# Performance work log

Hardware: AMD Instinct MI355X
Metric: run time of the kernel (lower is better)

Reference implementation:

```python
import jax, jax.numpy as jnp
import numpy as np


def _glorot(key, shape):
    lim = np.sqrt(6.0 / (shape[-2] + shape[-1])).astype(np.float32)
    return jax.random.uniform(key, shape, jnp.float32, -lim, lim)


def setup_inputs() -> dict:
    key = jax.random.key(0)
    B, F, K, L = 8192, 256, 32768, 4
    H = 2 * F          # CouplingLayer(feat_size, feat_size * 2) hidden width
    half = F // 2      # affine coupling transforms half the features
    ks = jax.random.split(key, 6)
    return {
        "inputs": jax.random.normal(ks[0], (B, F), jnp.float32),
        "W1": _glorot(ks[1], (L, half, H)),
        "b1": jnp.zeros((L, H), jnp.float32),
        "Ws": _glorot(ks[2], (L, H, half)),
        "bs": jnp.zeros((L, half), jnp.float32),
        "Wt": _glorot(ks[3], (L, H, half)),
        "bt": jnp.zeros((L, half), jnp.float32),
        "prior": _glorot(ks[4], (K, F)),  # VQ codebook, GlorotUniform init as in source
    }


def _forward_flow(x, W1, b1, Ws, bs, Wt, bt):
    """Stack of affine coupling layers; returns (y, log|det J|) per sample."""
    L = W1.shape[0]
    jac = jnp.zeros((x.shape[0],), x.dtype)
    for l in range(L):  # small fixed layer count
        xa, xb = jnp.split(x, 2, axis=1)                 # [B, F/2] each
        h = jax.nn.relu(xa @ W1[l] + b1[l])              # [B, 2F]
        s_raw = h @ Ws[l] + bs[l]                        # [B, F/2]
        s = s_raw if l == L - 1 else jnp.tanh(s_raw)     # last layer: tf.identity
        t = h @ Wt[l] + bt[l]
        yb = xb * jnp.exp(s) + t
        jac = jac + jnp.sum(s, axis=1)
        x = jnp.concatenate([yb, xa], axis=1)            # swap halves for mixing
    return x, jac


def reference(inputs, W1, b1, Ws, bs, Wt, bt, prior):
    sg = jax.lax.stop_gradient
    x, jac = _forward_flow(inputs, W1, b1, Ws, bs, Wt, bt)   # [B, F], [B]
    # pairwise squared distance to codebook: [B, K]
    na = jnp.sum(x * x, axis=1, keepdims=True)               # [B, 1]
    nb = jnp.sum(prior * prior, axis=1)[None, :]             # [1, K]
    d = jnp.maximum(na - 2.0 * (x @ prior.T) + nb, 0.0)      # [B, K]
    target_ind = jnp.argmin(d, axis=1)                       # [B]
    target = prior[target_ind]                               # gather, [B, F]
    loss_1 = jnp.mean(jnp.sum((x - sg(target)) ** 2, axis=1) / 2)
    loss_2 = jnp.mean(jnp.sum((sg(x) - target) ** 2, axis=1) / 2)
    loss = loss_1 + 0.25 * loss_2 - jnp.mean(jac)
    return x, loss
```

## Files before the change

kernel.cpp:

```cpp
#include <hip/hip_runtime.h>
#include <stdint.h>

#define NB     8192
#define NF     256
#define NHALF  128
#define NHID   512
#define NLAY   4
#define NK     32768

typedef __attribute__((ext_vector_type(8))) short bf16x8;
typedef __attribute__((ext_vector_type(4))) float f32x4;

static __device__ __forceinline__ unsigned short f2bf(float f) {
  union { float f; unsigned int u; } v; v.f = f;
  return (unsigned short)((v.u + 0x7FFFu + ((v.u >> 16) & 1u)) >> 16);
}
static __device__ __forceinline__ float bf2f(unsigned short u) {
  union { unsigned int u; float f; } v; v.u = ((unsigned int)u) << 16; return v.f;
}

static __device__ __forceinline__ void load_lds16(const void* g, void* l) {
  __builtin_amdgcn_global_load_lds(
      (const __attribute__((address_space(1))) unsigned int*)g,
      (__attribute__((address_space(3))) unsigned int*)l, 16, 0, 0);
}

static __device__ __forceinline__ unsigned long long packsi(float v, int idx) {
  unsigned int b = __float_as_uint(v);
  b = (b & 0x80000000u) ? ~b : (b | 0x80000000u);
  return ((unsigned long long)b << 32) | (unsigned int)(~(unsigned int)idx);
}

static __device__ __forceinline__ float fast_tanh(float x) {
  const float xc = fminf(fmaxf(x, -15.f), 15.f);
  const float e2 = __expf(2.f * xc);
  return 1.f - 2.f / (e2 + 1.f);
}

static __device__ __forceinline__ int swadr(int kseg, int nrows, int row, int kin) {
  return (kseg * nrows + row) * 64 + (((kin >> 3) ^ (row & 7)) * 8) + (kin & 7);
}

__global__ __launch_bounds__(256, 2)
void flow_all(const float* __restrict__ in,
              const unsigned short* __restrict__ W1T,
              const unsigned short* __restrict__ W2I,
              const float* __restrict__ b1A,
              const float* __restrict__ bsA,
              const float* __restrict__ btA,
              float* __restrict__ xout,
              unsigned short* __restrict__ xfbf,
              float* __restrict__ jac)
{
  __shared__ __align__(16) unsigned short Xb[2][16 * 128];
  __shared__ __align__(16) unsigned short Hs[2 * 16 * 64];
  __shared__ __align__(16) unsigned short Bs[2048 * 8];
  __shared__ float jlds[3][16];
  const int tid = threadIdx.x;
  const int lane = tid & 63, wave = tid >> 6;
  const int q = lane >> 4, c = lane & 15;
  const int m0 = blockIdx.x * 16;

#pragma unroll
  for (int v = 0; v < 4; v++) {
    const int t4 = tid + v * 256;
    const int row = t4 >> 6, f4 = t4 & 63;
    const float4 d = *(const float4*)(in + (size_t)(m0 + row) * NF + f4 * 4);
    unsigned short* dst = Xb[f4 >> 5];
    const int feat = (f4 & 31) * 4;
    const float vals[4] = {d.x, d.y, d.z, d.w};
#pragma unroll
    for (int u = 0; u < 4; u++) {
      const int fe = feat + u;
      dst[swadr(fe >> 6, 16, row, fe & 63)] = f2bf(vals[u]);
    }
  }

  float jr[4];
#pragma unroll
  for (int r = 0; r < 4; r++) jr[r] = 0.f;

  for (int l = 0; l < NLAY; l++) {
    __syncthreads();
    const unsigned short* W1l = W1T + (size_t)l * NHID * NHALF;
    const unsigned short* W2l = W2I + (size_t)l * NF * NHID;
    const float* b1l = b1A + l * NHID;
    const float* bsl = bsA + l * NHALF;
    const float* btl = btA + l * NHALF;
    unsigned short* XA = Xb[l & 1];
    unsigned short* XB = Xb[1 - (l & 1)];

    bf16x8 af1[4];
#pragma unroll
    for (int kw = 0; kw < 4; kw++) {
      const int kch = kw * 4 + q;
      af1[kw] = *(const bf16x8*)(XA + ((kch >> 3) * 16 + c) * 64 +
                                 (((kch & 7) ^ (c & 7)) * 8));
    }

    const f32x4 z = {0.f, 0.f, 0.f, 0.f};
    f32x4 acc2[4];
#pragma unroll
    for (int j = 0; j < 4; j++) acc2[j] = z;

    for (int nc = 0; nc < 4; nc++) {
      __syncthreads();
#pragma unroll
      for (int u = 0; u < 8; u++) {
        const int chb = (wave * 8 + u) * 64;
        const int ch = chb + lane;
        const int kseg = ch >> 10, cs = ch & 1023;
        const int row = cs >> 3, cc = (cs & 7) ^ (row & 7);
        load_lds16(W1l + (size_t)(nc * 128 + row) * NHALF + kseg * 64 + cc * 8,
                   Bs + chb * 8);
      }
      __syncthreads();

      f32x4 acc1[2];
#pragma unroll
      for (int j = 0; j < 2; j++) acc1[j] = z;

#pragma unroll
      for (int kw = 0; kw < 4; kw++) {
        const int kseg = kw >> 1, g = (kw & 1) * 4 + q;
#pragma unroll
        for (int j = 0; j < 2; j++) {
          const int rb = wave * 32 + 16 * j + c;
          const bf16x8 bf = *(const bf16x8*)(Bs + (kseg * 128 + rb) * 64 + ((g ^ (rb & 7)) * 8));
          acc1[j] = __builtin_amdgcn_mfma_f32_16x16x32_bf16(af1[kw], bf, acc1[j], 0, 0, 0);
        }
      }
#pragma unroll
      for (int j = 0; j < 2; j++) {
        const int hc = wave * 32 + 16 * j + c;
        const float bb = b1l[nc * 128 + hc];
#pragma unroll
        for (int r = 0; r < 4; r++) {
          float v = acc1[j][r] + bb;
          v = v > 0.f ? v : 0.f;
          Hs[swadr(hc >> 6, 16, 4 * q + r, hc & 63)] = f2bf(v);
        }
      }

      for (int kt2 = 0; kt2 < 2; kt2++) {
        __syncthreads();
#pragma unroll
        for (int u = 0; u < 8; u++) {
          const int chb = (wave * 8 + u) * 64;
          const int ch = chb + lane;
          const int row = ch >> 3, cc = (ch & 7) ^ (row & 7);
          load_lds16(W2l + (size_t)row * NHID + nc * 128 + kt2 * 64 + cc * 8,
                     Bs + chb * 8);
        }
        __syncthreads();
#pragma unroll
        for (int ks = 0; ks < 2; ks++) {
          const int g = ks * 4 + q;
          const bf16x8 afh = *(const bf16x8*)(Hs + (kt2 * 16 + c) * 64 + ((g ^ (c & 7)) * 8));
#pragma unroll
          for (int j = 0; j < 4; j++) {
            const int rb = wave * 64 + 16 * j + c;
            const bf16x8 bf = *(const bf16x8*)(Bs + rb * 64 + ((g ^ (rb & 7)) * 8));
            acc2[j] = __builtin_amdgcn_mfma_f32_16x16x32_bf16(afh, bf, acc2[j], 0, 0, 0);
          }
        }
      }
    }

    const int parity = c & 1;
    const int lastl = (l == NLAY - 1);
#pragma unroll
    for (int j = 0; j < 4; j++) {
      const int col = wave * 64 + 16 * j + c;
#pragma unroll
      for (int r = 0; r < 4; r++) {
        const float val = acc2[j][r];
        const float oth = __shfl_xor(val, 1);
        if (!parity) {
          const int feat = col >> 1;
          float s = val + bsl[feat];
          if (!lastl) s = fast_tanh(s);
          const float t = oth + btl[feat];
          const int row = 4 * q + r;
          const int xaddr = swadr(feat >> 6, 16, row, feat & 63);
          const float xb = bf2f(XB[xaddr]);
          const float yb = xb * __expf(s) + t;
          jr[r] += s;
          XB[xaddr] = f2bf(yb);
          const size_t grow = (size_t)(m0 + row) * NF;
          if (l == 2) { xout[grow + NHALF + feat] = yb; xfbf[grow + NHALF + feat] = f2bf(yb); }
          if (lastl)  { xout[grow + feat] = yb;         xfbf[grow + feat] = f2bf(yb); }
        }
      }
    }
  }

  float v0[4];
#pragma unroll
  for (int r = 0; r < 4; r++) {
    float v = jr[r];
    v += __shfl_xor(v, 1); v += __shfl_xor(v, 2);
    v += __shfl_xor(v, 4); v += __shfl_xor(v, 8);
    if (c == 0) {
      if (wave) jlds[wave - 1][4 * q + r] = v;
      else v0[r] = v;
    }
  }
  __syncthreads();
  if (wave == 0 && c == 0) {
#pragma unroll
    for (int r = 0; r < 4; r++) {
      const int row = 4 * q + r;
      jac[m0 + row] = v0[r] + jlds[0][row] + jlds[1][row] + jlds[2][row];
    }
  }
}

__global__ __launch_bounds__(256, 2)
void vq_argmax(const unsigned short* __restrict__ X,
               const unsigned short* __restrict__ P,
               const float* __restrict__ nbh,
               unsigned long long* __restrict__ gbest)
{
  __shared__ __align__(16) unsigned short Bs[4 * 64 * 64];
  const int tid = threadIdx.x;
  const int lane = tid & 63, wave = tid >> 6;
  const int y = blockIdx.x & 15;
  const int m0 = (blockIdx.x >> 4) * 256;
  const int q = lane >> 4, c = lane & 15;
  const int mw = m0 + wave * 64;

  bf16x8 af[4][8];
#pragma unroll
  for (int i = 0; i < 4; i++) {
    const unsigned short* xr = X + (size_t)(mw + 16 * i + c) * 256 + q * 8;
#pragma unroll
    for (int kc = 0; kc < 8; kc++) af[i][kc] = *(const bf16x8*)(xr + kc * 32);
  }

  float bestv[16];
  int besti[16];
#pragma unroll
  for (int t = 0; t < 16; t++) { bestv[t] = -1e30f; besti[t] = 0; }

  for (int nt = 0; nt < 32; nt++) {
    const int n0 = y * 2048 + nt * 64;
    if (nt) __syncthreads();
#pragma unroll
    for (int u = 0; u < 8; u++) {
      const int chb = (wave * 8 + u) * 64;
      const int ch = chb + lane;
      const int kseg = ch >> 9, cs = ch & 511;
      const int row = cs >> 3, cc = (cs & 7) ^ (row & 7);
      load_lds16(P + (size_t)(n0 + row) * 256 + kseg * 64 + cc * 8, Bs + chb * 8);
    }
    __syncthreads();

    const f32x4 z = {0.f, 0.f, 0.f, 0.f};
    f32x4 acc[4][4];
#pragma unroll
    for (int i = 0; i < 4; i++)
#pragma unroll
      for (int j = 0; j < 4; j++) acc[i][j] = z;

#pragma unroll
    for (int kseg = 0; kseg < 4; kseg++)
#pragma unroll
      for (int ks = 0; ks < 2; ks++) {
        const int kc = kseg * 2 + ks;
        const int g = ks * 4 + q;
#pragma unroll
        for (int j = 0; j < 4; j++) {
          const int rb = 16 * j + c;
          const bf16x8 bf = *(const bf16x8*)(Bs + (kseg * 64 + rb) * 64 + ((g ^ (rb & 7)) * 8));
          acc[0][j] = __builtin_amdgcn_mfma_f32_16x16x32_bf16(af[0][kc], bf, acc[0][j], 0, 0, 0);
          acc[1][j] = __builtin_amdgcn_mfma_f32_16x16x32_bf16(af[1][kc], bf, acc[1][j], 0, 0, 0);
          acc[2][j] = __builtin_amdgcn_mfma_f32_16x16x32_bf16(af[2][kc], bf, acc[2][j], 0, 0, 0);
          acc[3][j] = __builtin_amdgcn_mfma_f32_16x16x32_bf16(af[3][kc], bf, acc[3][j], 0, 0, 0);
        }
      }

#pragma unroll
    for (int j = 0; j < 4; j++) {
      const int col = n0 + 16 * j + c;
      const float nb = nbh[col];
#pragma unroll
      for (int i = 0; i < 4; i++)
#pragma unroll
        for (int r = 0; r < 4; r++) {
          const float sc = acc[i][j][r] - nb;
          const int t = i * 4 + r;
          if (sc > bestv[t]) { bestv[t] = sc; besti[t] = col; }
        }
    }
  }

#pragma unroll
  for (int t = 0; t < 16; t++) {
    float lv = bestv[t]; int li = besti[t];
#pragma unroll
    for (int mk = 8; mk >= 1; mk >>= 1) {
      const float ov = __shfl_xor(lv, mk);
      const int oi = __shfl_xor(li, mk);
      if (ov > lv || (ov == lv && oi < li)) { lv = ov; li = oi; }
    }
    if (c == 0) {
      const int row = mw + 16 * (t >> 2) + q * 4 + (t & 3);
      atomicMax(&gbest[row], packsi(lv, li));
    }
  }
}

__global__ void prep_all(const float* __restrict__ W1,
                         const float* __restrict__ Ws,
                         const float* __restrict__ Wt,
                         const float* __restrict__ prior,
                         unsigned short* __restrict__ W1T,
                         unsigned short* __restrict__ W2I,
                         unsigned short* __restrict__ pbf,
                         float* __restrict__ nbh,
                         unsigned long long* __restrict__ gbest,
                         float* __restrict__ accum)
{
  __shared__ float ts[64 * 65];
  const int bx = blockIdx.x;
  const int tid = threadIdx.x;
  if (bx < 2048) {
    const int k = bx * 16 + (tid >> 4);
    const int l16 = tid & 15;
    float s = 0.f;
#pragma unroll
    for (int v = 0; v < 4; v++) {
      const int off = (v * 16 + l16) * 4;
      const float4 d = *(const float4*)(prior + (size_t)k * NF + off);
      ushort4 o;
      o.x = f2bf(d.x); o.y = f2bf(d.y); o.z = f2bf(d.z); o.w = f2bf(d.w);
      *(ushort4*)(pbf + (size_t)k * NF + off) = o;
      s += d.x * d.x + d.y * d.y + d.z * d.z + d.w * d.w;
    }
#pragma unroll
    for (int mk = 8; mk >= 1; mk >>= 1) s += __shfl_xor(s, mk);
    if (l16 == 0) nbh[k] = 0.5f * s;
  } else if (bx < 2112) {
    const int job = bx - 2048;
    const int l = job >> 4, t = job & 15;
    const int k0 = (t >> 3) * 64, n0 = (t & 7) * 64;
    const float* src = W1 + (size_t)l * NHALF * NHID;
#pragma unroll
    for (int v = 0; v < 16; v++) {
      const int e = tid + v * 256;
      const int kk = e >> 6, nn = e & 63;
      ts[kk * 65 + nn] = src[(size_t)(k0 + kk) * NHID + n0 + nn];
    }
    __syncthreads();
    unsigned short* dst = W1T + (size_t)l * NHID * NHALF;
#pragma unroll
    for (int v = 0; v < 16; v++) {
      const int e = tid + v * 256;
      const int nn = e >> 6, kk = e & 63;
      dst[(size_t)(n0 + nn) * NHALF + k0 + kk] = f2bf(ts[kk * 65 + nn]);
    }
  } else if (bx < 2240) {
    const int job = bx - 2112;
    const int l = job >> 5, rem = job & 31;
    const int b = rem >> 4;
    const int k0 = ((rem >> 1) & 7) * 64;
    const int f0 = (rem & 1) * 64;
    const float* src = (b ? Wt : Ws) + (size_t)l * NHID * NHALF;
#pragma unroll
    for (int v = 0; v < 16; v++) {
      const int e = tid + v * 256;
      const int kk = e >> 6, nn = e & 63;
      ts[kk * 65 + nn] = src[(size_t)(k0 + kk) * NHALF + f0 + nn];
    }
    __syncthreads();
#pragma unroll
    for (int v = 0; v < 16; v++) {
      const int e = tid + v * 256;
      const int nn = e >> 6, kk = e & 63;
      W2I[((size_t)l * NF + 2 * (f0 + nn) + b) * NHID + k0 + kk] = f2bf(ts[kk * 65 + nn]);
    }
  } else {
    const int idx = (bx - 2240) * 256 + tid;
    if (idx < NB) gbest[idx] = 0ull;
    if (idx < 2) accum[idx] = 0.f;
  }
}

__global__ void vq_finalize(const float* __restrict__ X,
                            const float* __restrict__ prior,
                            const unsigned long long* __restrict__ gbest,
                            const float* __restrict__ jac,
                            float* __restrict__ accum)
{
  const int wave = threadIdx.x >> 6, lane = threadIdx.x & 63;
  const int gw = blockIdx.x * 4 + wave;
  float accd = 0.f, accj = 0.f;
  for (int r = 0; r < 8; r++) {
    const int row = gw * 8 + r;
    const unsigned int idx = ~(unsigned int)(gbest[row]);
    const float* x = X + (size_t)row * NF;
    const float* p = prior + (size_t)idx * NF;
#pragma unroll
    for (int u = 0; u < 4; u++) {
      const int d = lane + u * 64;
      const float df = x[d] - p[d];
      accd += df * df;
    }
    if (lane == 0) accj += jac[row];
  }
#pragma unroll
  for (int mk = 32; mk >= 1; mk >>= 1) {
    accd += __shfl_xor(accd, mk);
    accj += __shfl_xor(accj, mk);
  }
  __shared__ float sd[4], sj[4];
  if (lane == 0) { sd[wave] = accd; sj[wave] = accj; }
  __syncthreads();
  if (threadIdx.x == 0) {
    atomicAdd(&accum[0], sd[0] + sd[1] + sd[2] + sd[3]);
    atomicAdd(&accum[1], sj[0] + sj[1] + sj[2] + sj[3]);
  }
}

__global__ void finalize_loss(const float* __restrict__ acc, float* __restrict__ loss) {
  if (threadIdx.x == 0 && blockIdx.x == 0)
    loss[0] = 1.25f * (0.5f * acc[0] / (float)NB) - acc[1] / (float)NB;
}

extern "C" void kernel_launch(void* const* d_in, const int* in_sizes, int n_in,
                              void* d_out, int out_size, void* d_ws, size_t ws_size,
                              hipStream_t stream)
{
  (void)in_sizes; (void)n_in; (void)out_size; (void)ws_size;
  const float* inputs = (const float*)d_in[0];
  const float* W1 = (const float*)d_in[1];
  const float* b1 = (const float*)d_in[2];
  const float* Ws = (const float*)d_in[3];
  const float* bs = (const float*)d_in[4];
  const float* Wt = (const float*)d_in[5];
  const float* bt = (const float*)d_in[6];
  const float* prior = (const float*)d_in[7];

  char* p = (char*)d_ws;
  auto alloc = [&](size_t bytes) { char* r = p; p += (bytes + 255) & ~(size_t)255; return r; };
  unsigned short* W1T  = (unsigned short*)alloc((size_t)NLAY * NHID * NHALF * 2);
  unsigned short* W2I  = (unsigned short*)alloc((size_t)NLAY * NF * NHID * 2);
  unsigned short* PBF  = (unsigned short*)alloc((size_t)NK * NF * 2);
  float* NBH           = (float*)alloc((size_t)NK * 4);
  unsigned short* XFBF = (unsigned short*)alloc((size_t)NB * NF * 2);
  float* JAC           = (float*)alloc((size_t)NB * 4);
  unsigned long long* GBEST = (unsigned long long*)alloc((size_t)NB * 8);
  float* ACC           = (float*)alloc(256);

  float* xout = (float*)d_out;
  float* loss = xout + (size_t)NB * NF;

  prep_all<<<dim3(2272), 256, 0, stream>>>(
      W1, Ws, Wt, prior, W1T, W2I, PBF, NBH, GBEST, ACC);

  flow_all<<<dim3(NB / 16), 256, 0, stream>>>(
      inputs, W1T, W2I, b1, bs, bt, xout, XFBF, JAC);

  vq_argmax<<<dim3(32 * 16), 256, 0, stream>>>(XFBF, PBF, NBH, GBEST);
  vq_finalize<<<dim3(256), 256, 0, stream>>>(xout, prior, GBEST, JAC, ACC);
  finalize_loss<<<1, 1, 0, stream>>>(ACC, loss);
}
```

Before: 293.6 us.

## Use FP8 codebook distance GEMM and software-pipeline flow weight loads

The VQ distance GEMM switches from bf16 to fp8 e4m3 MFMA. Both the flow output and the codebook are scaled and quantized, with a K permutation so the 64-bit fragments load contiguously, which halves codebook bytes and doubles MFMA throughput. The flow kernel is restructured into a flat 96-step schedule with double-buffered LDS weight tiles, prefetching the next tile while the current one computes and cutting barriers. The risk is that fp8 precision flips argmin choices between close codebook entries, changing the selected targets and the loss.

```diff
diff --git a/kernel.cpp b/kernel.cpp
--- a/kernel.cpp
+++ b/kernel.cpp
@@ -1,4 +1,5 @@
 #include <hip/hip_runtime.h>
+#include <hip/hip_fp8.h>
 #include <stdint.h>
 
 #define NB     8192
@@ -8,8 +9,12 @@
 #define NLAY   4
 #define NK     32768
 
+#define SX     (1.0f / 16.0f)
+#define SP     (256.0f)
+
 typedef __attribute__((ext_vector_type(8))) short bf16x8;
 typedef __attribute__((ext_vector_type(4))) float f32x4;
+typedef __attribute__((ext_vector_type(2))) long i64x2;
 
 static __device__ __forceinline__ unsigned short f2bf(float f) {
   union { float f; unsigned int u; } v; v.f = f;
@@ -17,6 +22,16 @@
 }
 static __device__ __forceinline__ float bf2f(unsigned short u) {
   union { unsigned int u; float f; } v; v.u = ((unsigned int)u) << 16; return v.f;
+}
+static __device__ __forceinline__ unsigned char f2fp8(float f) {
+  __hip_fp8_e4m3 q(f);
+  return (unsigned char)q.__x;
+}
+static __device__ __forceinline__ float fp82f(unsigned char b) {
+  __hip_fp8_e4m3 q; q.__x = b; return (float)q;
+}
+static __device__ __forceinline__ int kperm(int k) {
+  return ((k >> 3) & 3) * 64 + ((k >> 5) << 3) + (k & 7);
 }
 
 static __device__ __forceinline__ void load_lds16(const void* g, void* l) {
@@ -49,17 +64,29 @@
               const float* __restrict__ bsA,
               const float* __restrict__ btA,
               float* __restrict__ xout,
-              unsigned short* __restrict__ xfbf,
+              unsigned char* __restrict__ xf8,
               float* __restrict__ jac)
 {
   __shared__ __align__(16) unsigned short Xb[2][16 * 128];
-  __shared__ __align__(16) unsigned short Hs[2 * 16 * 64];
-  __shared__ __align__(16) unsigned short Bs[2048 * 8];
+  __shared__ __align__(16) unsigned short Hs[16 * 64];
+  __shared__ __align__(16) unsigned short Bs[2][8192];
   __shared__ float jlds[3][16];
   const int tid = threadIdx.x;
   const int lane = tid & 63, wave = tid >> 6;
   const int q = lane >> 4, c = lane & 15;
   const int m0 = blockIdx.x * 16;
+
+  {
+    const unsigned short* W1l = W1T;
+#pragma unroll
+    for (int u = 0; u < 4; u++) {
+      const int chb = (u * 4 + wave) * 64;
+      const int ch = chb + lane;
+      const int kseg = ch >> 9, cs = ch & 511;
+      const int row = cs >> 3, cc = (cs & 7) ^ (row & 7);
+      load_lds16(W1l + (size_t)row * 128 + kseg * 64 + cc * 8, Bs[0] + chb * 8);
+    }
+  }
 
 #pragma unroll
   for (int v = 0; v < 4; v++) {
@@ -76,120 +103,114 @@
     }
   }
 
-  float jr[4];
-#pragma unroll
-  for (int r = 0; r < 4; r++) jr[r] = 0.f;
-
-  for (int l = 0; l < NLAY; l++) {
+  float jr[4] = {0.f, 0.f, 0.f, 0.f};
+  bf16x8 af1[4];
+  const f32x4 z = {0.f, 0.f, 0.f, 0.f};
+  f32x4 acc2[4];
+
+  for (int gs = 0; gs < 96; gs++) {
     __syncthreads();
-    const unsigned short* W1l = W1T + (size_t)l * NHID * NHALF;
-    const unsigned short* W2l = W2I + (size_t)l * NF * NHID;
-    const float* b1l = b1A + l * NHID;
-    const float* bsl = bsA + l * NHALF;
-    const float* btl = btA + l * NHALF;
+
+    if (gs + 1 < 96) {
+      const int g2 = gs + 1;
+      const int l2 = g2 / 24, s2 = g2 % 24, nc2 = s2 / 3, t2 = s2 % 3;
+      unsigned short* dst = Bs[g2 & 1];
+      if (t2 == 0) {
+        const unsigned short* W1l = W1T + (size_t)l2 * (NHID * NHALF) + (size_t)nc2 * 64 * 128;
+#pragma unroll
+        for (int u = 0; u < 4; u++) {
+          const int chb = (u * 4 + wave) * 64;
+          const int ch = chb + lane;
+          const int kseg = ch >> 9, cs = ch & 511;
+          const int row = cs >> 3, cc = (cs & 7) ^ (row & 7);
+          load_lds16(W1l + (size_t)row * 128 + kseg * 64 + cc * 8, dst + chb * 8);
+        }
+      } else {
+        const unsigned short* W2l = W2I + (size_t)l2 * (NF * NHID) + nc2 * 64 + (t2 - 1) * 32;
+#pragma unroll
+        for (int u = 0; u < 4; u++) {
+          const int chb = (u * 4 + wave) * 64;
+          const int ch = chb + lane;
+          const int row = ch >> 2;
+          const int cc = (ch & 3) ^ ((row >> 1) & 3);
+          load_lds16(W2l + (size_t)row * NHID + cc * 8, dst + chb * 8);
+        }
+      }
+    }
+
+    const int l = gs / 24, s = gs % 24, nc8 = s / 3, typ = s % 3;
+    const unsigned short* B = Bs[gs & 1];
     unsigned short* XA = Xb[l & 1];
     unsigned short* XB = Xb[1 - (l & 1)];
 
-    bf16x8 af1[4];
-#pragma unroll
-    for (int kw = 0; kw < 4; kw++) {
-      const int kch = kw * 4 + q;
-      af1[kw] = *(const bf16x8*)(XA + ((kch >> 3) * 16 + c) * 64 +
-                                 (((kch & 7) ^ (c & 7)) * 8));
-    }
-
-    const f32x4 z = {0.f, 0.f, 0.f, 0.f};
-    f32x4 acc2[4];
-#pragma unroll
-    for (int j = 0; j < 4; j++) acc2[j] = z;
-
-    for (int nc = 0; nc < 4; nc++) {
-      __syncthreads();
-#pragma unroll
-      for (int u = 0; u < 8; u++) {
-        const int chb = (wave * 8 + u) * 64;
-        const int ch = chb + lane;
-        const int kseg = ch >> 10, cs = ch & 1023;
-        const int row = cs >> 3, cc = (cs & 7) ^ (row & 7);
-        load_lds16(W1l + (size_t)(nc * 128 + row) * NHALF + kseg * 64 + cc * 8,
-                   Bs + chb * 8);
-      }
-      __syncthreads();
-
-      f32x4 acc1[2];
-#pragma unroll
-      for (int j = 0; j < 2; j++) acc1[j] = z;
-
+    if (typ == 0) {
+      if (s == 0) {
+#pragma unroll
+        for (int kw = 0; kw < 4; kw++) {
+          const int kch = kw * 4 + q;
+          af1[kw] = *(const bf16x8*)(XA + ((kch >> 3) * 16 + c) * 64 +
+                                     (((kch & 7) ^ (c & 7)) * 8));
+        }
+#pragma unroll
+        for (int j = 0; j < 4; j++) acc2[j] = z;
+      }
+      f32x4 acc1 = z;
+      const int rb = wave * 16 + c;
 #pragma unroll
       for (int kw = 0; kw < 4; kw++) {
         const int kseg = kw >> 1, g = (kw & 1) * 4 + q;
-#pragma unroll
-        for (int j = 0; j < 2; j++) {
-          const int rb = wave * 32 + 16 * j + c;
-          const bf16x8 bf = *(const bf16x8*)(Bs + (kseg * 128 + rb) * 64 + ((g ^ (rb & 7)) * 8));
-          acc1[j] = __builtin_amdgcn_mfma_f32_16x16x32_bf16(af1[kw], bf, acc1[j], 0, 0, 0);
-        }
-      }
-#pragma unroll
-      for (int j = 0; j < 2; j++) {
-        const int hc = wave * 32 + 16 * j + c;
-        const float bb = b1l[nc * 128 + hc];
+        const bf16x8 bf = *(const bf16x8*)(B + (kseg * 64 + rb) * 64 + ((g ^ (rb & 7)) * 8));
+        acc1 = __builtin_amdgcn_mfma_f32_16x16x32_bf16(af1[kw], bf, acc1, 0, 0, 0);
+      }
+      const int hc = wave * 16 + c;
+      const float bb = b1A[l * NHID + nc8 * 64 + hc];
+#pragma unroll
+      for (int r = 0; r < 4; r++) {
+        float v = acc1[r] + bb;
+        v = v > 0.f ? v : 0.f;
+        Hs[swadr(0, 16, 4 * q + r, hc)] = f2bf(v);
+      }
+    } else {
+      const int half = typ - 1;
+      const bf16x8 afh = *(const bf16x8*)(Hs + c * 64 + (((half * 4 + q) ^ (c & 7)) * 8));
+#pragma unroll
+      for (int j = 0; j < 4; j++) {
+        const int rb = wave * 64 + 16 * j + c;
+        const bf16x8 bf = *(const bf16x8*)(B + rb * 32 + ((q ^ ((rb >> 1) & 3)) * 8));
+        acc2[j] = __builtin_amdgcn_mfma_f32_16x16x32_bf16(afh, bf, acc2[j], 0, 0, 0);
+      }
+    }
+
+    if (s == 23) {
+      const int parity = c & 1;
+      const int lastl = (l == NLAY - 1);
+      const float* bsl = bsA + l * NHALF;
+      const float* btl = btA + l * NHALF;
+#pragma unroll
+      for (int j = 0; j < 4; j++) {
+        const int col = wave * 64 + 16 * j + c;
 #pragma unroll
         for (int r = 0; r < 4; r++) {
-          float v = acc1[j][r] + bb;
-          v = v > 0.f ? v : 0.f;
-          Hs[swadr(hc >> 6, 16, 4 * q + r, hc & 63)] = f2bf(v);
-        }
-      }
-
-      for (int kt2 = 0; kt2 < 2; kt2++) {
-        __syncthreads();
-#pragma unroll
-        for (int u = 0; u < 8; u++) {
-          const int chb = (wave * 8 + u) * 64;
-          const int ch = chb + lane;
-          const int row = ch >> 3, cc = (ch & 7) ^ (row & 7);
-          load_lds16(W2l + (size_t)row * NHID + nc * 128 + kt2 * 64 + cc * 8,
-                     Bs + chb * 8);
-        }
-        __syncthreads();
-#pragma unroll
-        for (int ks = 0; ks < 2; ks++) {
-          const int g = ks * 4 + q;
-          const bf16x8 afh = *(const bf16x8*)(Hs + (kt2 * 16 + c) * 64 + ((g ^ (c & 7)) * 8));
-#pragma unroll
-          for (int j = 0; j < 4; j++) {
-            const int rb = wave * 64 + 16 * j + c;
-            const bf16x8 bf = *(const bf16x8*)(Bs + rb * 64 + ((g ^ (rb & 7)) * 8));
-            acc2[j] = __builtin_amdgcn_mfma_f32_16x16x32_bf16(afh, bf, acc2[j], 0, 0, 0);
+          const float val = acc2[j][r];
+          const float oth = __shfl_xor(val, 1);
+          if (!parity) {
+            const int feat = col >> 1;
+            float sv = val + bsl[feat];
+            if (!lastl) sv = fast_tanh(sv);
+            const float t = oth + btl[feat];
+            const int row = 4 * q + r;
+            const int xaddr = swadr(feat >> 6, 16, row, feat & 63);
+            const float xb = bf2f(XB[xaddr]);
+            const float yb = xb * __expf(sv) + t;
+            jr[r] += sv;
+            XB[xaddr] = f2bf(yb);
+            if (l >= 2) {
+              const int k = lastl ? feat : (NHALF + feat);
+              const size_t grow = (size_t)(m0 + row) * NF;
+              xout[grow + k] = yb;
+              xf8[(size_t)(m0 + row) * 256 + kperm(k)] = f2fp8(yb * SX);
+            }
           }
-        }
-      }
-    }
-
-    const int parity = c & 1;
-    const int lastl = (l == NLAY - 1);
-#pragma unroll
-    for (int j = 0; j < 4; j++) {
-      const int col = wave * 64 + 16 * j + c;
-#pragma unroll
-      for (int r = 0; r < 4; r++) {
-        const float val = acc2[j][r];
-        const float oth = __shfl_xor(val, 1);
-        if (!parity) {
-          const int feat = col >> 1;
-          float s = val + bsl[feat];
-          if (!lastl) s = fast_tanh(s);
-          const float t = oth + btl[feat];
-          const int row = 4 * q + r;
-          const int xaddr = swadr(feat >> 6, 16, row, feat & 63);
-          const float xb = bf2f(XB[xaddr]);
-          const float yb = xb * __expf(s) + t;
-          jr[r] += s;
-          XB[xaddr] = f2bf(yb);
-          const size_t grow = (size_t)(m0 + row) * NF;
-          if (l == 2) { xout[grow + NHALF + feat] = yb; xfbf[grow + NHALF + feat] = f2bf(yb); }
-          if (lastl)  { xout[grow + feat] = yb;         xfbf[grow + feat] = f2bf(yb); }
         }
       }
     }
@@ -217,12 +238,12 @@
 }
 
 __global__ __launch_bounds__(256, 2)
-void vq_argmax(const unsigned short* __restrict__ X,
-               const unsigned short* __restrict__ P,
+void vq_argmax(const unsigned char* __restrict__ X8,
+               const unsigned char* __restrict__ P8,
                const float* __restrict__ nbh,
                unsigned long long* __restrict__ gbest)
 {
-  __shared__ __align__(16) unsigned short Bs[4 * 64 * 64];
+  __shared__ __align__(16) unsigned char Bs[64 * 256];
   const int tid = threadIdx.x;
   const int lane = tid & 63, wave = tid >> 6;
   const int y = blockIdx.x & 15;
@@ -230,12 +251,15 @@
   const int q = lane >> 4, c = lane & 15;
   const int mw = m0 + wave * 64;
 
-  bf16x8 af[4][8];
+  long af[4][8];
 #pragma unroll
   for (int i = 0; i < 4; i++) {
-    const unsigned short* xr = X + (size_t)(mw + 16 * i + c) * 256 + q * 8;
-#pragma unroll
-    for (int kc = 0; kc < 8; kc++) af[i][kc] = *(const bf16x8*)(xr + kc * 32);
+    const unsigned char* xr = X8 + (size_t)(mw + 16 * i + c) * 256 + q * 64;
+#pragma unroll
+    for (int kc2 = 0; kc2 < 4; kc2++) {
+      const i64x2 v = *(const i64x2*)(xr + kc2 * 16);
+      af[i][2 * kc2] = v.x; af[i][2 * kc2 + 1] = v.y;
+    }
   }
 
   float bestv[16];
@@ -247,12 +271,12 @@
     const int n0 = y * 2048 + nt * 64;
     if (nt) __syncthreads();
 #pragma unroll
-    for (int u = 0; u < 8; u++) {
-      const int chb = (wave * 8 + u) * 64;
+    for (int u = 0; u < 4; u++) {
+      const int chb = (u * 4 + wave) * 64;
       const int ch = chb + lane;
-      const int kseg = ch >> 9, cs = ch & 511;
-      const int row = cs >> 3, cc = (cs & 7) ^ (row & 7);
-      load_lds16(P + (size_t)(n0 + row) * 256 + kseg * 64 + cc * 8, Bs + chb * 8);
+      const int row = ch >> 4, gslot = ch & 15;
+      load_lds16(P8 + (size_t)(n0 + row) * 256 + (gslot ^ (row & 15)) * 16,
+                 Bs + chb * 16);
     }
     __syncthreads();
 
@@ -264,21 +288,19 @@
       for (int j = 0; j < 4; j++) acc[i][j] = z;
 
 #pragma unroll
-    for (int kseg = 0; kseg < 4; kseg++)
-#pragma unroll
-      for (int ks = 0; ks < 2; ks++) {
-        const int kc = kseg * 2 + ks;
-        const int g = ks * 4 + q;
-#pragma unroll
-        for (int j = 0; j < 4; j++) {
-          const int rb = 16 * j + c;
-          const bf16x8 bf = *(const bf16x8*)(Bs + (kseg * 64 + rb) * 64 + ((g ^ (rb & 7)) * 8));
-          acc[0][j] = __builtin_amdgcn_mfma_f32_16x16x32_bf16(af[0][kc], bf, acc[0][j], 0, 0, 0);
-          acc[1][j] = __builtin_amdgcn_mfma_f32_16x16x32_bf16(af[1][kc], bf, acc[1][j], 0, 0, 0);
-          acc[2][j] = __builtin_amdgcn_mfma_f32_16x16x32_bf16(af[2][kc], bf, acc[2][j], 0, 0, 0);
-          acc[3][j] = __builtin_amdgcn_mfma_f32_16x16x32_bf16(af[3][kc], bf, acc[3][j], 0, 0, 0);
-        }
-      }
+    for (int kc2 = 0; kc2 < 4; kc2++) {
+      const int g = q * 4 + kc2;
+#pragma unroll
+      for (int j = 0; j < 4; j++) {
+        const int rb = 16 * j + c;
+        const i64x2 b2 = *(const i64x2*)(Bs + rb * 256 + ((g ^ (rb & 15)) * 16));
+#pragma unroll
+        for (int i = 0; i < 4; i++) {
+          acc[i][j] = __builtin_amdgcn_mfma_f32_16x16x32_fp8_fp8(af[i][2 * kc2],     b2.x, acc[i][j], 0, 0, 0);
+          acc[i][j] = __builtin_amdgcn_mfma_f32_16x16x32_fp8_fp8(af[i][2 * kc2 + 1], b2.y, acc[i][j], 0, 0, 0);
+        }
+      }
+    }
 
 #pragma unroll
     for (int j = 0; j < 4; j++) {
@@ -317,7 +339,7 @@
                          const float* __restrict__ prior,
                          unsigned short* __restrict__ W1T,
                          unsigned short* __restrict__ W2I,
-                         unsigned short* __restrict__ pbf,
+                         unsigned char* __restrict__ p8,
                          float* __restrict__ nbh,
                          unsigned long long* __restrict__ gbest,
                          float* __restrict__ accum)
@@ -333,14 +355,16 @@
     for (int v = 0; v < 4; v++) {
       const int off = (v * 16 + l16) * 4;
       const float4 d = *(const float4*)(prior + (size_t)k * NF + off);
-      ushort4 o;
-      o.x = f2bf(d.x); o.y = f2bf(d.y); o.z = f2bf(d.z); o.w = f2bf(d.w);
-      *(ushort4*)(pbf + (size_t)k * NF + off) = o;
-      s += d.x * d.x + d.y * d.y + d.z * d.z + d.w * d.w;
+      uchar4 o;
+      o.x = f2fp8(d.x * SP); o.y = f2fp8(d.y * SP);
+      o.z = f2fp8(d.z * SP); o.w = f2fp8(d.w * SP);
+      *(uchar4*)(p8 + (size_t)k * 256 + kperm(off)) = o;
+      const float q0 = fp82f(o.x), q1 = fp82f(o.y), q2 = fp82f(o.z), q3 = fp82f(o.w);
+      s += q0 * q0 + q1 * q1 + q2 * q2 + q3 * q3;
     }
 #pragma unroll
     for (int mk = 8; mk >= 1; mk >>= 1) s += __shfl_xor(s, mk);
-    if (l16 == 0) nbh[k] = 0.5f * s;
+    if (l16 == 0) nbh[k] = 0.5f * s * (SX / SP);
   } else if (bx < 2112) {
     const int job = bx - 2048;
     const int l = job >> 4, t = job & 15;
@@ -446,9 +470,9 @@
   auto alloc = [&](size_t bytes) { char* r = p; p += (bytes + 255) & ~(size_t)255; return r; };
   unsigned short* W1T  = (unsigned short*)alloc((size_t)NLAY * NHID * NHALF * 2);
   unsigned short* W2I  = (unsigned short*)alloc((size_t)NLAY * NF * NHID * 2);
-  unsigned short* PBF  = (unsigned short*)alloc((size_t)NK * NF * 2);
+  unsigned char* P8    = (unsigned char*)alloc((size_t)NK * 256);
   float* NBH           = (float*)alloc((size_t)NK * 4);
-  unsigned short* XFBF = (unsigned short*)alloc((size_t)NB * NF * 2);
+  unsigned char* XF8   = (unsigned char*)alloc((size_t)NB * 256);
   float* JAC           = (float*)alloc((size_t)NB * 4);
   unsigned long long* GBEST = (unsigned long long*)alloc((size_t)NB * 8);
   float* ACC           = (float*)alloc(256);
@@ -457,12 +481,12 @@
   float* loss = xout + (size_t)NB * NF;
 
   prep_all<<<dim3(2272), 256, 0, stream>>>(
-      W1, Ws, Wt, prior, W1T, W2I, PBF, NBH, GBEST, ACC);
+      W1, Ws, Wt, prior, W1T, W2I, P8, NBH, GBEST, ACC);
 
   flow_all<<<dim3(NB / 16), 256, 0, stream>>>(
-      inputs, W1T, W2I, b1, bs, bt, xout, XFBF, JAC);
-
-  vq_argmax<<<dim3(32 * 16), 256, 0, stream>>>(XFBF, PBF, NBH, GBEST);
+      inputs, W1T, W2I, b1, bs, bt, xout, XF8, JAC);
+
+  vq_argmax<<<dim3(32 * 16), 256, 0, stream>>>(XF8, P8, NBH, GBEST);
   vq_finalize<<<dim3(256), 256, 0, stream>>>(xout, prior, GBEST, JAC, ACC);
   finalize_loss<<<1, 1, 0, stream>>>(ACC, loss);
 }
```

New measurement: 291.8 us. About the same (-0.6%).
